# Kernel optimization log

Measured on AMD Instinct MI355X. Metric: run time of the kernel, lower is better.

## Reference

```python
import jax, jax.numpy as jnp
import numpy as np

NEG_SLOPE = 0.2


def _gat_layer(x, src, dst, n, W, a_src, a_dst, b, concat):
    """PyG-style GATConv (inference, self-loops already in src/dst).
    x: [N, Fin]; W: [Fin, H*C]; a_src/a_dst: [H, C]; b: [H*C] or [C]."""
    H, C = a_src.shape
    h = (x @ W).reshape(-1, H, C)                      # [N, H, C]
    al_s = jnp.einsum('nhc,hc->nh', h, a_src)          # [N, H]
    al_d = jnp.einsum('nhc,hc->nh', h, a_dst)          # [N, H]
    e = al_s[src] + al_d[dst]                          # [E, H]
    e = jnp.where(e >= 0, e, NEG_SLOPE * e)            # LeakyReLU(0.2)
    m = jax.ops.segment_max(e, dst, num_segments=n)    # [N, H] softmax over dst
    e = jnp.exp(e - m[dst])
    s = jax.ops.segment_sum(e, dst, num_segments=n)    # [N, H]
    alpha = e / (s[dst] + 1e-16)                       # [E, H]
    msg = h[src] * alpha[:, :, None]                   # [E, H, C]
    out = jax.ops.segment_sum(msg, dst, num_segments=n)  # [N, H, C]
    if concat:
        out = out.reshape(-1, H * C)
    else:
        out = out.mean(axis=1)
    return out + b


def _forward(x, edge_index, W1, as1, ad1, b1, W2, as2, ad2, b2, W3, as3, ad3, b3):
    n = x.shape[0]
    loops = jnp.arange(n, dtype=edge_index.dtype)
    src = jnp.concatenate([edge_index[0], loops])      # add self-loops (PyG default)
    dst = jnp.concatenate([edge_index[1], loops])
    x = _gat_layer(x, src, dst, n, W1, as1, ad1, b1, concat=True)
    x = jax.nn.elu(x)
    x = _gat_layer(x, src, dst, n, W2, as2, ad2, b2, concat=True)
    x = jax.nn.elu(x)
    x = _gat_layer(x, src, dst, n, W3, as3, ad3, b3, concat=False)
    return x


def setup_inputs() -> dict:
    key = jax.random.key(0)
    ks = jax.random.split(key, 16)
    N, E, FIN, HID, H, OUT = 50000, 320000, 256, 64, 4, 64
    sc = 0.1  # keep attention logits in a sane range
    return {
        'x': jax.random.normal(ks[0], (N, FIN), jnp.float32),
        'edge_index': jax.random.randint(ks[1], (2, E), 0, N, jnp.int32),
        'W1': jax.random.normal(ks[2], (FIN, H * HID), jnp.float32) * sc,
        'as1': jax.random.normal(ks[3], (H, HID), jnp.float32) * sc,
        'ad1': jax.random.normal(ks[4], (H, HID), jnp.float32) * sc,
        'b1': jax.random.normal(ks[5], (H * HID,), jnp.float32) * sc,
        'W2': jax.random.normal(ks[6], (H * HID, H * HID), jnp.float32) * sc,
        'as2': jax.random.normal(ks[7], (H, HID), jnp.float32) * sc,
        'ad2': jax.random.normal(ks[8], (H, HID), jnp.float32) * sc,
        'b2': jax.random.normal(ks[9], (H * HID,), jnp.float32) * sc,
        'W3': jax.random.normal(ks[10], (H * HID, OUT), jnp.float32) * sc,
        'as3': jax.random.normal(ks[11], (1, OUT), jnp.float32) * sc,
        'ad3': jax.random.normal(ks[12], (1, OUT), jnp.float32) * sc,
        'b3': jax.random.normal(ks[13], (OUT,), jnp.float32) * sc,
    }


def reference(x, edge_index, W1, as1, ad1, b1, W2, as2, ad2, b2, W3, as3, ad3, b3):
    return _forward(x, edge_index, W1, as1, ad1, b1, W2, as2, ad2, b2, W3, as3, ad3, b3)
```

## Files before the change

### kernel.cpp

```cpp
#include <hip/hip_runtime.h>


typedef __attribute__((ext_vector_type(8))) __bf16 bf16x8;
typedef __attribute__((ext_vector_type(4))) float f32x4;
typedef _Float16 f16x8 __attribute__((ext_vector_type(8)));
typedef _Float16 f16x4 __attribute__((ext_vector_type(4)));

#define NEG_SLOPE 0.2f
#define WELL 40

__device__ __forceinline__ unsigned short f2b_rne(float f) {
    unsigned int u = __float_as_uint(f);
    u += 0x7FFFu + ((u >> 16) & 1u);
    return (unsigned short)(u >> 16);
}
__device__ __forceinline__ unsigned short f2h(float f) {
    _Float16 h = (_Float16)f;
    unsigned short s;
    __builtin_memcpy(&s, &h, 2);
    return s;
}
__device__ __forceinline__ bf16x8 cvt8(const float* f) {
    unsigned short r[8];
#pragma unroll
    for (int j = 0; j < 8; j++) r[j] = f2b_rne(f[j]);
    bf16x8 v;
    __builtin_memcpy(&v, r, 16);
    return v;
}
__device__ __forceinline__ float lrelu(float e) {
    return e >= 0.f ? e : NEG_SLOPE * e;
}

__global__ __launch_bounds__(256) void k_init(const float* __restrict__ W1,
                                              const float* __restrict__ W2,
                                              const float* __restrict__ W3,
                                              unsigned short* __restrict__ W1t,
                                              unsigned short* __restrict__ W2t,
                                              unsigned short* __restrict__ W3t,
                                              int* __restrict__ cnt, int n) {
    int t = blockIdx.x * blockDim.x + threadIdx.x;
    if (t < n) cnt[t] = 0;
    const float* W;
    unsigned short* Wt;
    int Nout, idx = t;
    if (idx < 65536)        { W = W1; Wt = W1t; Nout = 256; }
    else if (idx < 131072)  { W = W2; Wt = W2t; Nout = 256; idx -= 65536; }
    else if (idx < 147456)  { W = W3; Wt = W3t; Nout = 64;  idx -= 131072; }
    else return;
    int k = idx / Nout;
    int c = idx - k * Nout;
    Wt[(size_t)c * 256 + k] = f2b_rne(W[idx]);
}

__global__ __launch_bounds__(256) void k_fillell(const int* __restrict__ src,
                                                 const int* __restrict__ dst,
                                                 int* __restrict__ cnt,
                                                 int* __restrict__ ell, int E) {
    int t = blockIdx.x * blockDim.x + threadIdx.x;
    if (t < E) {
        int d = dst[t];
        int pos = atomicAdd(&cnt[d], 1);
        if (pos < WELL) ell[(size_t)d * WELL + pos] = src[t];
    }
}

template <int NT, bool AF32>
__global__ __launch_bounds__(512) void k_gemm(const void* __restrict__ Av,
                                              const __bf16* __restrict__ Bt,
                                              unsigned short* __restrict__ h16,
                                              float* __restrict__ als,
                                              float* __restrict__ ald,
                                              const float* __restrict__ a_s,
                                              const float* __restrict__ a_d,
                                              int M, int H) {
    constexpr int NN = NT * 16;
    __shared__ __align__(16) __bf16 Bs[NN][256];

    const int tid = threadIdx.x;
    const int lane = tid & 63;
    const int w = tid >> 6;
    const int i = lane & 15;
    const int quad = lane >> 4;
    const int m0 = blockIdx.x * 256;

    {
        int nl = lane >> 5;
        int p = lane & 31;
#pragma unroll
        for (int t = 0; t < NN / 16; t++) {
            int n = t * 16 + w * 2 + nl;
            int g = p ^ (n & 7);
            const __bf16* gp = Bt + (size_t)n * 256 + g * 8;
            __builtin_amdgcn_global_load_lds(
                (const __attribute__((address_space(1))) void*)gp,
                (__attribute__((address_space(3))) void*)&Bs[t * 16 + w * 2][0],
                16, 0, 0);
        }
    }

    int ra = m0 + w * 32 + i;
    int rb = ra + 16;
    if (ra >= M) ra = M - 1;
    if (rb >= M) rb = M - 1;

    bf16x8 afrag[2][8];
    if (AF32) {
        const float* pa = (const float*)Av + (size_t)ra * 256;
        const float* pb = (const float*)Av + (size_t)rb * 256;
#pragma unroll
        for (int half = 0; half < 2; half++) {
            float tmp[2][4][8];
#pragma unroll
            for (int k4 = 0; k4 < 4; k4++) {
                int koff = (half * 4 + k4) * 32 + quad * 8;
                *(float4*)&tmp[0][k4][0] = *(const float4*)(pa + koff);
                *(float4*)&tmp[0][k4][4] = *(const float4*)(pa + koff + 4);
                *(float4*)&tmp[1][k4][0] = *(const float4*)(pb + koff);
                *(float4*)&tmp[1][k4][4] = *(const float4*)(pb + koff + 4);
            }
#pragma unroll
            for (int k4 = 0; k4 < 4; k4++) {
                afrag[0][half * 4 + k4] = cvt8(tmp[0][k4]);
                afrag[1][half * 4 + k4] = cvt8(tmp[1][k4]);
            }
        }
    } else {
        const __bf16* pa = (const __bf16*)Av + (size_t)ra * 256;
        const __bf16* pb = (const __bf16*)Av + (size_t)rb * 256;
#pragma unroll
        for (int kc = 0; kc < 8; kc++) {
            int koff = kc * 32 + quad * 8;
            afrag[0][kc] = *(const bf16x8*)(pa + koff);
            afrag[1][kc] = *(const bf16x8*)(pb + koff);
        }
    }

    f32x4 acc[2][NT] = {};

    __syncthreads();

#pragma unroll
    for (int kc = 0; kc < 8; kc++) {
        const int c = kc * 4 + quad;
#pragma unroll
        for (int nt = 0; nt < NT; nt++) {
            const int n = nt * 16 + i;
            const int p = c ^ (n & 7);
            bf16x8 bfv = *(const bf16x8*)&Bs[n][p * 8];
            acc[0][nt] = __builtin_amdgcn_mfma_f32_16x16x32_bf16(
                afrag[0][kc], bfv, acc[0][nt], 0, 0, 0);
            acc[1][nt] = __builtin_amdgcn_mfma_f32_16x16x32_bf16(
                afrag[1][kc], bfv, acc[1][nt], 0, 0, 0);
        }
    }

    float asv[NT], adv[NT];
#pragma unroll
    for (int nt = 0; nt < NT; nt++) {
        asv[nt] = a_s[(nt / 4) * 64 + (nt & 3) * 16 + i];
        adv[nt] = a_d[(nt / 4) * 64 + (nt & 3) * 16 + i];
    }

#pragma unroll
    for (int mt = 0; mt < 2; mt++) {
#pragma unroll
        for (int r = 0; r < 4; r++) {
            int row = m0 + w * 32 + mt * 16 + quad * 4 + r;
            bool ok = row < M;
#pragma unroll
            for (int nt = 0; nt < NT; nt++) {
                if (ok) h16[(size_t)row * NN + nt * 16 + i] = f2h(acc[mt][nt][r]);
            }
#pragma unroll
            for (int g = 0; g < (NT + 3) / 4; g++) {
                float ps = 0.f, pd = 0.f;
#pragma unroll
                for (int j = 0; j < 4 && g * 4 + j < NT; j++) {
                    float v = acc[mt][g * 4 + j][r];
                    ps += v * asv[g * 4 + j];
                    pd += v * adv[g * 4 + j];
                }
#pragma unroll
                for (int off = 1; off <= 8; off <<= 1) {
                    ps += __shfl_xor(ps, off, 64);
                    pd += __shfl_xor(pd, off, 64);
                }
                if (ok && i == 0) {
                    als[(size_t)row * H + g] = ps;
                    ald[(size_t)row * H + g] = pd;
                }
            }
        }
    }
}

__global__ __launch_bounds__(256) void k_agg4(const unsigned short* __restrict__ h16,
                                              const float* __restrict__ als,
                                              const float* __restrict__ ald,
                                              const int* __restrict__ cnt,
                                              const int* __restrict__ ell,
                                              const float* __restrict__ bias,
                                              unsigned short* __restrict__ xout,
                                              int n) {
    int gw = (blockIdx.x * blockDim.x + threadIdx.x) >> 6;
    int lane = threadIdx.x & 63;
    int wid = gw * 4 + (lane >> 4);
    if (wid >= n) return;
    int l = lane & 15;
    int head = l >> 2;
    int ch = l * 16;
    int base = lane & 48;

    int deg = min(cnt[wid], WELL);
    const int* row = ell + (size_t)wid * WELL;
    int myid = (l < deg) ? row[l] : 0;

    float aldv = ald[wid * 4 + head];
    float p = __expf(fminf(lrelu(als[wid * 4 + head] + aldv), 60.f));
    float ssum = p;
    float a[16];
    {
        f16x8 h0 = *(const f16x8*)&h16[(size_t)wid * 256 + ch];
        f16x8 h1 = *(const f16x8*)&h16[(size_t)wid * 256 + ch + 8];
#pragma unroll
        for (int j = 0; j < 8; j++) { a[j] = p * (float)h0[j]; a[8 + j] = p * (float)h1[j]; }
    }

    int jmax = min(deg, 16);
    int dm1 = deg - 1;
    for (int j = 0; j < jmax; j += 4) {
        int s0 = __shfl(myid, base + min(j, dm1));
        int s1 = __shfl(myid, base + min(j + 1, dm1));
        int s2 = __shfl(myid, base + min(j + 2, dm1));
        int s3 = __shfl(myid, base + min(j + 3, dm1));
        float e0 = als[s0 * 4 + head];
        float e1 = als[s1 * 4 + head];
        float e2 = als[s2 * 4 + head];
        float e3 = als[s3 * 4 + head];
        f16x8 v0a = *(const f16x8*)&h16[(size_t)s0 * 256 + ch];
        f16x8 v0b = *(const f16x8*)&h16[(size_t)s0 * 256 + ch + 8];
        f16x8 v1a = *(const f16x8*)&h16[(size_t)s1 * 256 + ch];
        f16x8 v1b = *(const f16x8*)&h16[(size_t)s1 * 256 + ch + 8];
        f16x8 v2a = *(const f16x8*)&h16[(size_t)s2 * 256 + ch];
        f16x8 v2b = *(const f16x8*)&h16[(size_t)s2 * 256 + ch + 8];
        f16x8 v3a = *(const f16x8*)&h16[(size_t)s3 * 256 + ch];
        f16x8 v3b = *(const f16x8*)&h16[(size_t)s3 * 256 + ch + 8];
        float p0 = __expf(fminf(lrelu(e0 + aldv), 60.f));
        float p1 = (j + 1 < deg) ? __expf(fminf(lrelu(e1 + aldv), 60.f)) : 0.f;
        float p2 = (j + 2 < deg) ? __expf(fminf(lrelu(e2 + aldv), 60.f)) : 0.f;
        float p3 = (j + 3 < deg) ? __expf(fminf(lrelu(e3 + aldv), 60.f)) : 0.f;
        ssum += (p0 + p1) + (p2 + p3);
#pragma unroll
        for (int k = 0; k < 8; k++) {
            a[k]     += (p0 * (float)v0a[k] + p1 * (float)v1a[k]) +
                        (p2 * (float)v2a[k] + p3 * (float)v3a[k]);
            a[8 + k] += (p0 * (float)v0b[k] + p1 * (float)v1b[k]) +
                        (p2 * (float)v2b[k] + p3 * (float)v3b[k]);
        }
    }
    for (int j = 16; j < deg; ++j) {
        int s0 = row[j];
        float p0 = __expf(fminf(lrelu(als[s0 * 4 + head] + aldv), 60.f));
        f16x8 v0a = *(const f16x8*)&h16[(size_t)s0 * 256 + ch];
        f16x8 v0b = *(const f16x8*)&h16[(size_t)s0 * 256 + ch + 8];
        ssum += p0;
#pragma unroll
        for (int k = 0; k < 8; k++) {
            a[k] += p0 * (float)v0a[k];
            a[8 + k] += p0 * (float)v0b[k];
        }
    }

    float inv = 1.f / (ssum + 1e-16f);
    float bb[16];
#pragma unroll
    for (int q = 0; q < 4; q++)
        *(float4*)&bb[q * 4] = *(const float4*)&bias[ch + q * 4];
    unsigned short o[16];
#pragma unroll
    for (int k = 0; k < 16; k++) {
        float r = a[k] * inv + bb[k];
        r = r > 0.f ? r : expm1f(r);
        o[k] = f2b_rne(r);
    }
    *(int4*)&xout[(size_t)wid * 256 + ch] = *(const int4*)&o[0];
    *(int4*)&xout[(size_t)wid * 256 + ch + 8] = *(const int4*)&o[8];
}

__global__ __launch_bounds__(256) void k_agg1(const unsigned short* __restrict__ h16,
                                              const float* __restrict__ als,
                                              const float* __restrict__ ald,
                                              const int* __restrict__ cnt,
                                              const int* __restrict__ ell,
                                              const float* __restrict__ bias,
                                              float* __restrict__ out, int n) {
    int gw = (blockIdx.x * blockDim.x + threadIdx.x) >> 6;
    int lane = threadIdx.x & 63;
    int wid = gw * 4 + (lane >> 4);
    if (wid >= n) return;
    int l = lane & 15;
    int ch = l * 4;
    int base = lane & 48;

    int deg = min(cnt[wid], WELL);
    const int* row = ell + (size_t)wid * WELL;
    int myid = (l < deg) ? row[l] : 0;

    float aldv = ald[wid];
    float p = __expf(fminf(lrelu(als[wid] + aldv), 60.f));
    float ssum = p;
    float a[4];
    {
        f16x4 hv = *(const f16x4*)&h16[(size_t)wid * 64 + ch];
#pragma unroll
        for (int k = 0; k < 4; k++) a[k] = p * (float)hv[k];
    }

    int jmax = min(deg, 16);
    int dm1 = deg - 1;
    for (int j = 0; j < jmax; j += 4) {
        int s0 = __shfl(myid, base + min(j, dm1));
        int s1 = __shfl(myid, base + min(j + 1, dm1));
        int s2 = __shfl(myid, base + min(j + 2, dm1));
        int s3 = __shfl(myid, base + min(j + 3, dm1));
        float e0 = als[s0], e1 = als[s1], e2 = als[s2], e3 = als[s3];
        f16x4 v0 = *(const f16x4*)&h16[(size_t)s0 * 64 + ch];
        f16x4 v1 = *(const f16x4*)&h16[(size_t)s1 * 64 + ch];
        f16x4 v2 = *(const f16x4*)&h16[(size_t)s2 * 64 + ch];
        f16x4 v3 = *(const f16x4*)&h16[(size_t)s3 * 64 + ch];
        float p0 = __expf(fminf(lrelu(e0 + aldv), 60.f));
        float p1 = (j + 1 < deg) ? __expf(fminf(lrelu(e1 + aldv), 60.f)) : 0.f;
        float p2 = (j + 2 < deg) ? __expf(fminf(lrelu(e2 + aldv), 60.f)) : 0.f;
        float p3 = (j + 3 < deg) ? __expf(fminf(lrelu(e3 + aldv), 60.f)) : 0.f;
        ssum += (p0 + p1) + (p2 + p3);
#pragma unroll
        for (int k = 0; k < 4; k++)
            a[k] += (p0 * (float)v0[k] + p1 * (float)v1[k]) +
                    (p2 * (float)v2[k] + p3 * (float)v3[k]);
    }
    for (int j = 16; j < deg; ++j) {
        int s0 = row[j];
        float p0 = __expf(fminf(lrelu(als[s0] + aldv), 60.f));
        f16x4 v0 = *(const f16x4*)&h16[(size_t)s0 * 64 + ch];
        ssum += p0;
#pragma unroll
        for (int k = 0; k < 4; k++) a[k] += p0 * (float)v0[k];
    }
    float inv = 1.f / (ssum + 1e-16f);
    float4 bv = *(const float4*)&bias[ch];
    float4 r;
    r.x = a[0] * inv + bv.x;
    r.y = a[1] * inv + bv.y;
    r.z = a[2] * inv + bv.z;
    r.w = a[3] * inv + bv.w;
    *(float4*)&out[(size_t)wid * 64 + ch] = r;
}

extern "C" void kernel_launch(void* const* d_in, const int* in_sizes, int n_in,
                              void* d_out, int out_size, void* d_ws, size_t ws_size,
                              hipStream_t stream) {
    const float* x   = (const float*)d_in[0];
    const int*   ei  = (const int*)d_in[1];
    const float* W1  = (const float*)d_in[2];
    const float* as1 = (const float*)d_in[3];
    const float* ad1 = (const float*)d_in[4];
    const float* b1  = (const float*)d_in[5];
    const float* W2  = (const float*)d_in[6];
    const float* as2 = (const float*)d_in[7];
    const float* ad2 = (const float*)d_in[8];
    const float* b2  = (const float*)d_in[9];
    const float* W3  = (const float*)d_in[10];
    const float* as3 = (const float*)d_in[11];
    const float* ad3 = (const float*)d_in[12];
    const float* b3  = (const float*)d_in[13];

    const int N = in_sizes[0] / 256;
    const int E = in_sizes[1] / 2;

    size_t off = 0;
    auto alloc = [&](size_t bytes) -> void* {
        void* p = (char*)d_ws + off;
        off += (bytes + 255) & ~(size_t)255;
        return p;
    };
    unsigned short* xb  = (unsigned short*)alloc((size_t)N * 256 * 2);
    unsigned short* W1t = (unsigned short*)alloc((size_t)256 * 256 * 2);
    unsigned short* W2t = (unsigned short*)alloc((size_t)256 * 256 * 2);
    unsigned short* W3t = (unsigned short*)alloc((size_t)64 * 256 * 2);
    unsigned short* h16 = (unsigned short*)alloc((size_t)N * 256 * 2);
    float* als = (float*)alloc((size_t)N * 4 * 4);
    float* ald = (float*)alloc((size_t)N * 4 * 4);
    int* cnt   = (int*)alloc((size_t)N * 4);
    int* ell   = (int*)alloc((size_t)N * WELL * 4);

    const int T = 256;
    const int agg_blocks = (N + 15) / 16;
    const int mtiles = (N + 255) / 256;

    k_init<<<dim3(576), T, 0, stream>>>(W1, W2, W3, W1t, W2t, W3t, cnt, N);

    k_fillell<<<dim3((E + T - 1) / T), T, 0, stream>>>(ei, ei + E, cnt, ell, E);

    k_gemm<16, true><<<dim3(mtiles), 512, 0, stream>>>(x, (const __bf16*)W1t,
                                                       h16, als, ald, as1, ad1, N, 4);
    k_agg4<<<dim3(agg_blocks), T, 0, stream>>>(h16, als, ald, cnt, ell, b1, xb, N);

    k_gemm<16, false><<<dim3(mtiles), 512, 0, stream>>>(xb, (const __bf16*)W2t,
                                                        h16, als, ald, as2, ad2, N, 4);
    k_agg4<<<dim3(agg_blocks), T, 0, stream>>>(h16, als, ald, cnt, ell, b2, xb, N);

    k_gemm<4, false><<<dim3(mtiles), 512, 0, stream>>>(xb, (const __bf16*)W3t,
                                                       h16, als, ald, as3, ad3, N, 1);
    k_agg1<<<dim3(agg_blocks), T, 0, stream>>>(h16, als, ald, cnt, ell, b3,
                                               (float*)d_out, N);
}
```

Before: 267.2 us.

## Fuse ELL fill into first GEMM and remap aggregation lanes per node

The separate edge-to-ELL fill kernel is folded into the first GEMM launch: 60 extra blocks run the atomic fill with a grid-stride loop while the GEMM blocks compute, which removes one launch and overlaps the two. The 4-head aggregation now gives each node 32 lanes with 8 channels each, instead of 16 lanes with 16 channels, so the shuffle-fed unrolled loop covers up to 32 neighbours. The single-head aggregation now gives each node 8 lanes with 8 channels each and reads neighbour ids from memory past the first 8. These mappings trade more lanes per node and more blocks for lower register use and wider per-lane loads.

```diff
diff --git a/kernel.cpp b/kernel.cpp
--- a/kernel.cpp
+++ b/kernel.cpp
@@ -53,19 +53,7 @@
     Wt[(size_t)c * 256 + k] = f2b_rne(W[idx]);
 }
 
-__global__ __launch_bounds__(256) void k_fillell(const int* __restrict__ src,
-                                                 const int* __restrict__ dst,
-                                                 int* __restrict__ cnt,
-                                                 int* __restrict__ ell, int E) {
-    int t = blockIdx.x * blockDim.x + threadIdx.x;
-    if (t < E) {
-        int d = dst[t];
-        int pos = atomicAdd(&cnt[d], 1);
-        if (pos < WELL) ell[(size_t)d * WELL + pos] = src[t];
-    }
-}
-
-template <int NT, bool AF32>
+template <int NT, bool AF32, bool FILL>
 __global__ __launch_bounds__(512) void k_gemm(const void* __restrict__ Av,
                                               const __bf16* __restrict__ Bt,
                                               unsigned short* __restrict__ h16,
@@ -73,9 +61,25 @@
                                               float* __restrict__ ald,
                                               const float* __restrict__ a_s,
                                               const float* __restrict__ a_d,
-                                              int M, int H) {
+                                              int M, int H,
+                                              const int* __restrict__ esrc,
+                                              const int* __restrict__ edst,
+                                              int* __restrict__ cnt,
+                                              int* __restrict__ ell,
+                                              int E, int mtiles) {
     constexpr int NN = NT * 16;
     __shared__ __align__(16) __bf16 Bs[NN][256];
+
+    if (FILL && (int)blockIdx.x >= mtiles) {
+        int t = ((int)blockIdx.x - mtiles) * (int)blockDim.x + (int)threadIdx.x;
+        int stride = ((int)gridDim.x - mtiles) * (int)blockDim.x;
+        for (; t < E; t += stride) {
+            int d = edst[t];
+            int pos = atomicAdd(&cnt[d], 1);
+            if (pos < WELL) ell[(size_t)d * WELL + pos] = esrc[t];
+        }
+        return;
+    }
 
     const int tid = threadIdx.x;
     const int lane = tid & 63;
@@ -205,12 +209,12 @@
                                               int n) {
     int gw = (blockIdx.x * blockDim.x + threadIdx.x) >> 6;
     int lane = threadIdx.x & 63;
-    int wid = gw * 4 + (lane >> 4);
+    int wid = gw * 2 + (lane >> 5);
     if (wid >= n) return;
-    int l = lane & 15;
-    int head = l >> 2;
-    int ch = l * 16;
-    int base = lane & 48;
+    int l = lane & 31;
+    int head = l >> 3;
+    int ch = l * 8;
+    int base = lane & 32;
 
     int deg = min(cnt[wid], WELL);
     const int* row = ell + (size_t)wid * WELL;
@@ -219,15 +223,14 @@
     float aldv = ald[wid * 4 + head];
     float p = __expf(fminf(lrelu(als[wid * 4 + head] + aldv), 60.f));
     float ssum = p;
-    float a[16];
+    float a[8];
     {
         f16x8 h0 = *(const f16x8*)&h16[(size_t)wid * 256 + ch];
-        f16x8 h1 = *(const f16x8*)&h16[(size_t)wid * 256 + ch + 8];
-#pragma unroll
-        for (int j = 0; j < 8; j++) { a[j] = p * (float)h0[j]; a[8 + j] = p * (float)h1[j]; }
-    }
-
-    int jmax = min(deg, 16);
+#pragma unroll
+        for (int j = 0; j < 8; j++) a[j] = p * (float)h0[j];
+    }
+
+    int jmax = min(deg, 32);
     int dm1 = deg - 1;
     for (int j = 0; j < jmax; j += 4) {
         int s0 = __shfl(myid, base + min(j, dm1));
@@ -238,14 +241,10 @@
         float e1 = als[s1 * 4 + head];
         float e2 = als[s2 * 4 + head];
         float e3 = als[s3 * 4 + head];
-        f16x8 v0a = *(const f16x8*)&h16[(size_t)s0 * 256 + ch];
-        f16x8 v0b = *(const f16x8*)&h16[(size_t)s0 * 256 + ch + 8];
-        f16x8 v1a = *(const f16x8*)&h16[(size_t)s1 * 256 + ch];
-        f16x8 v1b = *(const f16x8*)&h16[(size_t)s1 * 256 + ch + 8];
-        f16x8 v2a = *(const f16x8*)&h16[(size_t)s2 * 256 + ch];
-        f16x8 v2b = *(const f16x8*)&h16[(size_t)s2 * 256 + ch + 8];
-        f16x8 v3a = *(const f16x8*)&h16[(size_t)s3 * 256 + ch];
-        f16x8 v3b = *(const f16x8*)&h16[(size_t)s3 * 256 + ch + 8];
+        f16x8 v0 = *(const f16x8*)&h16[(size_t)s0 * 256 + ch];
+        f16x8 v1 = *(const f16x8*)&h16[(size_t)s1 * 256 + ch];
+        f16x8 v2 = *(const f16x8*)&h16[(size_t)s2 * 256 + ch];
+        f16x8 v3 = *(const f16x8*)&h16[(size_t)s3 * 256 + ch];
         float p0 = __expf(fminf(lrelu(e0 + aldv), 60.f));
         float p1 = (j + 1 < deg) ? __expf(fminf(lrelu(e1 + aldv), 60.f)) : 0.f;
         float p2 = (j + 2 < deg) ? __expf(fminf(lrelu(e2 + aldv), 60.f)) : 0.f;
@@ -253,39 +252,31 @@
         ssum += (p0 + p1) + (p2 + p3);
 #pragma unroll
         for (int k = 0; k < 8; k++) {
-            a[k]     += (p0 * (float)v0a[k] + p1 * (float)v1a[k]) +
-                        (p2 * (float)v2a[k] + p3 * (float)v3a[k]);
-            a[8 + k] += (p0 * (float)v0b[k] + p1 * (float)v1b[k]) +
-                        (p2 * (float)v2b[k] + p3 * (float)v3b[k]);
-        }
-    }
-    for (int j = 16; j < deg; ++j) {
+            a[k] += (p0 * (float)v0[k] + p1 * (float)v1[k]) +
+                    (p2 * (float)v2[k] + p3 * (float)v3[k]);
+        }
+    }
+    for (int j = 32; j < deg; ++j) {
         int s0 = row[j];
         float p0 = __expf(fminf(lrelu(als[s0 * 4 + head] + aldv), 60.f));
-        f16x8 v0a = *(const f16x8*)&h16[(size_t)s0 * 256 + ch];
-        f16x8 v0b = *(const f16x8*)&h16[(size_t)s0 * 256 + ch + 8];
+        f16x8 v0 = *(const f16x8*)&h16[(size_t)s0 * 256 + ch];
         ssum += p0;
 #pragma unroll
-        for (int k = 0; k < 8; k++) {
-            a[k] += p0 * (float)v0a[k];
-            a[8 + k] += p0 * (float)v0b[k];
-        }
+        for (int k = 0; k < 8; k++) a[k] += p0 * (float)v0[k];
     }
 
     float inv = 1.f / (ssum + 1e-16f);
-    float bb[16];
-#pragma unroll
-    for (int q = 0; q < 4; q++)
-        *(float4*)&bb[q * 4] = *(const float4*)&bias[ch + q * 4];
-    unsigned short o[16];
-#pragma unroll
-    for (int k = 0; k < 16; k++) {
+    float bb[8];
+    *(float4*)&bb[0] = *(const float4*)&bias[ch];
+    *(float4*)&bb[4] = *(const float4*)&bias[ch + 4];
+    unsigned short o[8];
+#pragma unroll
+    for (int k = 0; k < 8; k++) {
         float r = a[k] * inv + bb[k];
         r = r > 0.f ? r : expm1f(r);
         o[k] = f2b_rne(r);
     }
     *(int4*)&xout[(size_t)wid * 256 + ch] = *(const int4*)&o[0];
-    *(int4*)&xout[(size_t)wid * 256 + ch + 8] = *(const int4*)&o[8];
 }
 
 __global__ __launch_bounds__(256) void k_agg1(const unsigned short* __restrict__ h16,
@@ -297,11 +288,11 @@
                                               float* __restrict__ out, int n) {
     int gw = (blockIdx.x * blockDim.x + threadIdx.x) >> 6;
     int lane = threadIdx.x & 63;
-    int wid = gw * 4 + (lane >> 4);
+    int wid = gw * 8 + (lane >> 3);
     if (wid >= n) return;
-    int l = lane & 15;
-    int ch = l * 4;
-    int base = lane & 48;
+    int l = lane & 7;
+    int ch = l * 8;
+    int base = lane & 56;
 
     int deg = min(cnt[wid], WELL);
     const int* row = ell + (size_t)wid * WELL;
@@ -310,51 +301,51 @@
     float aldv = ald[wid];
     float p = __expf(fminf(lrelu(als[wid] + aldv), 60.f));
     float ssum = p;
-    float a[4];
+    float a[8];
     {
-        f16x4 hv = *(const f16x4*)&h16[(size_t)wid * 64 + ch];
-#pragma unroll
-        for (int k = 0; k < 4; k++) a[k] = p * (float)hv[k];
-    }
-
-    int jmax = min(deg, 16);
+        f16x8 hv = *(const f16x8*)&h16[(size_t)wid * 64 + ch];
+#pragma unroll
+        for (int k = 0; k < 8; k++) a[k] = p * (float)hv[k];
+    }
+
     int dm1 = deg - 1;
-    for (int j = 0; j < jmax; j += 4) {
-        int s0 = __shfl(myid, base + min(j, dm1));
-        int s1 = __shfl(myid, base + min(j + 1, dm1));
-        int s2 = __shfl(myid, base + min(j + 2, dm1));
-        int s3 = __shfl(myid, base + min(j + 3, dm1));
+    for (int j = 0; j < deg; j += 4) {
+        int i0 = min(j, dm1), i1 = min(j + 1, dm1);
+        int i2 = min(j + 2, dm1), i3 = min(j + 3, dm1);
+        int s0, s1, s2, s3;
+        if (j < 8) {
+            s0 = __shfl(myid, base + i0);
+            s1 = __shfl(myid, base + i1);
+            s2 = __shfl(myid, base + i2);
+            s3 = __shfl(myid, base + i3);
+        } else {
+            s0 = row[i0]; s1 = row[i1]; s2 = row[i2]; s3 = row[i3];
+        }
         float e0 = als[s0], e1 = als[s1], e2 = als[s2], e3 = als[s3];
-        f16x4 v0 = *(const f16x4*)&h16[(size_t)s0 * 64 + ch];
-        f16x4 v1 = *(const f16x4*)&h16[(size_t)s1 * 64 + ch];
-        f16x4 v2 = *(const f16x4*)&h16[(size_t)s2 * 64 + ch];
-        f16x4 v3 = *(const f16x4*)&h16[(size_t)s3 * 64 + ch];
+        f16x8 v0 = *(const f16x8*)&h16[(size_t)s0 * 64 + ch];
+        f16x8 v1 = *(const f16x8*)&h16[(size_t)s1 * 64 + ch];
+        f16x8 v2 = *(const f16x8*)&h16[(size_t)s2 * 64 + ch];
+        f16x8 v3 = *(const f16x8*)&h16[(size_t)s3 * 64 + ch];
         float p0 = __expf(fminf(lrelu(e0 + aldv), 60.f));
         float p1 = (j + 1 < deg) ? __expf(fminf(lrelu(e1 + aldv), 60.f)) : 0.f;
         float p2 = (j + 2 < deg) ? __expf(fminf(lrelu(e2 + aldv), 60.f)) : 0.f;
         float p3 = (j + 3 < deg) ? __expf(fminf(lrelu(e3 + aldv), 60.f)) : 0.f;
         ssum += (p0 + p1) + (p2 + p3);
 #pragma unroll
-        for (int k = 0; k < 4; k++)
+        for (int k = 0; k < 8; k++)
             a[k] += (p0 * (float)v0[k] + p1 * (float)v1[k]) +
                     (p2 * (float)v2[k] + p3 * (float)v3[k]);
     }
-    for (int j = 16; j < deg; ++j) {
-        int s0 = row[j];
-        float p0 = __expf(fminf(lrelu(als[s0] + aldv), 60.f));
-        f16x4 v0 = *(const f16x4*)&h16[(size_t)s0 * 64 + ch];
-        ssum += p0;
-#pragma unroll
-        for (int k = 0; k < 4; k++) a[k] += p0 * (float)v0[k];
-    }
+
     float inv = 1.f / (ssum + 1e-16f);
-    float4 bv = *(const float4*)&bias[ch];
-    float4 r;
-    r.x = a[0] * inv + bv.x;
-    r.y = a[1] * inv + bv.y;
-    r.z = a[2] * inv + bv.z;
-    r.w = a[3] * inv + bv.w;
-    *(float4*)&out[(size_t)wid * 64 + ch] = r;
+    float bb[8];
+    *(float4*)&bb[0] = *(const float4*)&bias[ch];
+    *(float4*)&bb[4] = *(const float4*)&bias[ch + 4];
+    float r[8];
+#pragma unroll
+    for (int k = 0; k < 8; k++) r[k] = a[k] * inv + bb[k];
+    *(float4*)&out[(size_t)wid * 64 + ch] = *(const float4*)&r[0];
+    *(float4*)&out[(size_t)wid * 64 + ch + 4] = *(const float4*)&r[4];
 }
 
 extern "C" void kernel_launch(void* const* d_in, const int* in_sizes, int n_in,
@@ -395,23 +386,25 @@
     int* ell   = (int*)alloc((size_t)N * WELL * 4);
 
     const int T = 256;
-    const int agg_blocks = (N + 15) / 16;
+    const int agg4_blocks = (N + 7) / 8;
+    const int agg1_blocks = (N + 31) / 32;
     const int mtiles = (N + 255) / 256;
 
     k_init<<<dim3(576), T, 0, stream>>>(W1, W2, W3, W1t, W2t, W3t, cnt, N);
 
-    k_fillell<<<dim3((E + T - 1) / T), T, 0, stream>>>(ei, ei + E, cnt, ell, E);
-
-    k_gemm<16, true><<<dim3(mtiles), 512, 0, stream>>>(x, (const __bf16*)W1t,
-                                                       h16, als, ald, as1, ad1, N, 4);
-    k_agg4<<<dim3(agg_blocks), T, 0, stream>>>(h16, als, ald, cnt, ell, b1, xb, N);
-
-    k_gemm<16, false><<<dim3(mtiles), 512, 0, stream>>>(xb, (const __bf16*)W2t,
-                                                        h16, als, ald, as2, ad2, N, 4);
-    k_agg4<<<dim3(agg_blocks), T, 0, stream>>>(h16, als, ald, cnt, ell, b2, xb, N);
-
-    k_gemm<4, false><<<dim3(mtiles), 512, 0, stream>>>(xb, (const __bf16*)W3t,
-                                                       h16, als, ald, as3, ad3, N, 1);
-    k_agg1<<<dim3(agg_blocks), T, 0, stream>>>(h16, als, ald, cnt, ell, b3,
-                                               (float*)d_out, N);
-}
+    k_gemm<16, true, true><<<dim3(mtiles + 60), 512, 0, stream>>>(
+        x, (const __bf16*)W1t, h16, als, ald, as1, ad1, N, 4,
+        ei, ei + E, cnt, ell, E, mtiles);
+    k_agg4<<<dim3(agg4_blocks), T, 0, stream>>>(h16, als, ald, cnt, ell, b1, xb, N);
+
+    k_gemm<16, false, false><<<dim3(mtiles), 512, 0, stream>>>(
+        xb, (const __bf16*)W2t, h16, als, ald, as2, ad2, N, 4,
+        nullptr, nullptr, nullptr, nullptr, 0, mtiles);
+    k_agg4<<<dim3(agg4_blocks), T, 0, stream>>>(h16, als, ald, cnt, ell, b2, xb, N);
+
+    k_gemm<4, false, false><<<dim3(mtiles), 512, 0, stream>>>(
+        xb, (const __bf16*)W3t, h16, als, ald, as3, ad3, N, 1,
+        nullptr, nullptr, nullptr, nullptr, 0, mtiles);
+    k_agg1<<<dim3(agg1_blocks), T, 0, stream>>>(h16, als, ald, cnt, ell, b3,
+                                                (float*)d_out, N);
+}
```

Measured after the change: 253.6 us. 5.1% less time.
